# Kernel tuning notes

Measured on AMD Instinct MI355X. Metric: run time of the kernel, lower is better.

Reference implementation:

```python
import jax, jax.numpy as jnp
import numpy as np

EMBED_DIM = 1024
NUM_HEADS = 16
HEAD_DIM = EMBED_DIM // NUM_HEADS
NUM_FEATS = 256
YAT_EPS = 0.1
BATCH = 4
SEQ = 4096


def setup_inputs() -> dict:
    key = jax.random.key(0)
    ks = jax.random.split(key, 6)
    s = 1.0 / np.sqrt(EMBED_DIM)
    return {
        "x": jax.random.normal(ks[0], (BATCH, SEQ, EMBED_DIM), jnp.float32),
        "Wq": jax.random.normal(ks[1], (EMBED_DIM, EMBED_DIM), jnp.float32) * s,
        "bq": jnp.zeros((EMBED_DIM,), jnp.float32),
        "Wk": jax.random.normal(ks[2], (EMBED_DIM, EMBED_DIM), jnp.float32) * s,
        "bk": jnp.zeros((EMBED_DIM,), jnp.float32),
        "Wv": jax.random.normal(ks[3], (EMBED_DIM, EMBED_DIM), jnp.float32) * s,
        "bv": jnp.zeros((EMBED_DIM,), jnp.float32),
        "Wo": jax.random.normal(ks[4], (EMBED_DIM, EMBED_DIM), jnp.float32) * s,
        "bo": jnp.zeros((EMBED_DIM,), jnp.float32),
        "projection": jax.random.normal(ks[5], (NUM_HEADS, NUM_FEATS, HEAD_DIM), jnp.float32),
    }


def _spherical_features(x, projection):
    # x: (b, h, s, d) -> (b, h, s, f)
    x_norm = x / (jnp.linalg.norm(x, axis=-1, keepdims=True) + 1e-8)
    proj = jnp.einsum('bhsd,hfd->bhsf', x_norm, projection)
    return jax.nn.relu(proj) + YAT_EPS


def reference(x, Wq, bq, Wk, bk, Wv, bv, Wo, bo, projection):
    b, s, _ = x.shape
    def heads(t):
        return jnp.transpose(t.reshape(b, s, NUM_HEADS, HEAD_DIM), (0, 2, 1, 3))
    Q = heads(x @ Wq + bq)
    K = heads(x @ Wk + bk)
    V = heads(x @ Wv + bv)
    Qp = _spherical_features(Q, projection)  # (b,h,s,f)
    Kp = _spherical_features(K, projection)
    KV = jnp.einsum('bhsf,bhsd->bhfd', Kp, V)           # (b,h,f,d)
    QKV = jnp.einsum('bhsf,bhfd->bhsd', Qp, KV)          # (b,h,s,d)
    K_sum = jnp.sum(Kp, axis=2)                          # (b,h,f)
    normalizer = jnp.einsum('bhsf,bhf->bhs', Qp, K_sum)[..., None]
    normalizer = jnp.maximum(normalizer, 1e-6)
    out = QKV / normalizer
    out = jnp.transpose(out, (0, 2, 1, 3)).reshape(b, s, EMBED_DIM)
    return out @ Wo + bo
```

## Files before the change

kernel.cpp:

```cpp
#include <hip/hip_runtime.h>
#include <stdint.h>

typedef __bf16 bf16_t;
typedef __bf16 bf16x4 __attribute__((ext_vector_type(4)));
typedef __bf16 bf16x8 __attribute__((ext_vector_type(8)));
typedef float  f32x4  __attribute__((ext_vector_type(4)));

typedef __attribute__((address_space(1))) const uint32_t gas_u32;
typedef __attribute__((address_space(3))) uint32_t las_u32;

#define MFMA16(a, b, c) __builtin_amdgcn_mfma_f32_16x16x32_bf16((a), (b), (c), 0, 0, 0)

__device__ __forceinline__ void gl_lds16(const bf16_t* g, bf16_t* l) {
    __builtin_amdgcn_global_load_lds((gas_u32*)g, (las_u32*)l, 16, 0, 0);
}

__global__ __launch_bounds__(256) void castbf(const float* __restrict__ X,
                                              bf16_t* __restrict__ Xb)
{
    size_t i = ((size_t)blockIdx.x * 256 + threadIdx.x) * 8;
    float4 a = *(const float4*)&X[i];
    float4 b = *(const float4*)&X[i + 4];
    bf16x8 o;
    o[0] = (bf16_t)a.x; o[1] = (bf16_t)a.y; o[2] = (bf16_t)a.z; o[3] = (bf16_t)a.w;
    o[4] = (bf16_t)b.x; o[5] = (bf16_t)b.y; o[6] = (bf16_t)b.z; o[7] = (bf16_t)b.w;
    *(bf16x8*)&Xb[i] = o;
}

__global__ __launch_bounds__(256) void ktrans(
    const float* __restrict__ W0, const float* __restrict__ W1,
    const float* __restrict__ W2, const float* __restrict__ W3,
    bf16_t* __restrict__ WT)
{
    __shared__ float t[64 * 68];
    const int z = blockIdx.z;
    const float* W = (z == 0) ? W0 : (z == 1) ? W1 : (z == 2) ? W2 : W3;
    bf16_t* O = WT + (size_t)z * 1024 * 1024;
    const int r0 = blockIdx.y * 64, c0 = blockIdx.x * 64;
    const int tid = threadIdx.x;
    const int row = tid >> 2, colg = (tid & 3) * 16;
#pragma unroll
    for (int p = 0; p < 4; ++p)
        *(float4*)&t[row * 68 + colg + p * 4] =
            *(const float4*)&W[(size_t)(r0 + row) * 1024 + c0 + colg + p * 4];
    __syncthreads();
    bf16x8 v0, v1;
#pragma unroll
    for (int j = 0; j < 8; ++j) {
        v0[j] = (bf16_t)t[(colg + j) * 68 + row];
        v1[j] = (bf16_t)t[(colg + 8 + j) * 68 + row];
    }
    *(bf16x8*)&O[(size_t)(c0 + row) * 1024 + r0 + colg] = v0;
    *(bf16x8*)&O[(size_t)(c0 + row) * 1024 + r0 + colg + 8] = v1;
}

template <int CMODE, typename OutT>
__global__ __launch_bounds__(256) void gemm_bt(
    const bf16_t* __restrict__ A, const bf16_t* __restrict__ Bt,
    const float* __restrict__ b0, const float* __restrict__ b1,
    const float* __restrict__ b2, OutT* __restrict__ C,
    int M, int N, int K)
{
    __shared__ bf16_t As[128 * 32];
    __shared__ bf16_t Bs[128 * 32];
    __shared__ bf16_t Cs[4][32 * 72];
    const int tid = threadIdx.x;
    const int lane = tid & 63, wave = tid >> 6;
    const int q = lane >> 4, ln = lane & 15;
    const int m0 = blockIdx.x * 128, n0 = blockIdx.y * 128;
    const int wm = (wave >> 1) * 64, wn = (wave & 1) * 64;
    const int srow = tid >> 2, scol = (tid & 3) * 8;

    f32x4 acc[4][4] = {};
    const bf16_t* Ag = A + (size_t)(m0 + srow) * K + scol;
    const bf16_t* Bg = Bt + (size_t)(n0 + srow) * K + scol;
    bf16_t* Al = As + srow * 32 + scol;
    bf16_t* Bl = Bs + srow * 32 + scol;

    for (int k0 = 0; k0 < K; k0 += 32) {
        __syncthreads();
        gl_lds16(Ag + k0, Al);
        gl_lds16(Ag + k0 + (size_t)64 * K, Al + 64 * 32);
        gl_lds16(Bg + k0, Bl);
        gl_lds16(Bg + k0 + (size_t)64 * K, Bl + 64 * 32);
        __syncthreads();
        bf16x8 a[4], b[4];
#pragma unroll
        for (int mt = 0; mt < 4; ++mt)
            a[mt] = *(const bf16x8*)&As[(wm + mt * 16 + ln) * 32 + q * 8];
#pragma unroll
        for (int nt = 0; nt < 4; ++nt)
            b[nt] = *(const bf16x8*)&Bs[(wn + nt * 16 + ln) * 32 + q * 8];
#pragma unroll
        for (int mt = 0; mt < 4; ++mt)
#pragma unroll
            for (int nt = 0; nt < 4; ++nt)
                acc[mt][nt] = MFMA16(a[mt], b[nt], acc[mt][nt]);
    }

    if (CMODE == 0) {
        float* myCf = (float*)&Cs[wave][0];
#pragma unroll
        for (int p = 0; p < 4; ++p) {
#pragma unroll
            for (int nt = 0; nt < 4; ++nt) {
                float bv = b0[n0 + wn + nt * 16 + ln];
#pragma unroll
                for (int r = 0; r < 4; ++r)
                    myCf[(q * 4 + r) * 68 + nt * 16 + ln] = acc[p][nt][r] + bv;
            }
#pragma unroll
            for (int c = 0; c < 4; ++c) {
                int flat = c * 64 + lane;
                int rr = flat >> 4, co = (flat & 15) * 4;
                f32x4 v = *(const f32x4*)&myCf[rr * 68 + co];
                *(f32x4*)&C[(size_t)(m0 + wm + p * 16 + rr) * N + n0 + wn + co] = v;
            }
        }
    } else {
        const int n_first = n0 + wn;
        const int t = n_first >> 10;
        const int h = (n_first >> 6) & 15;
        const float* bp = (t == 0) ? b0 : (t == 1) ? b1 : b2;
        const int m = m0 + wm;
        const int bI = m >> 12, s0 = m & 4095;
        bf16_t* Cp = (bf16_t*)C + (size_t)t * 16777216 + (size_t)(bI * 16 + h) * 262144;
        bf16_t* myCs = &Cs[wave][0];
#pragma unroll
        for (int p = 0; p < 2; ++p) {
#pragma unroll
            for (int mh = 0; mh < 2; ++mh) {
                int mt = p * 2 + mh;
#pragma unroll
                for (int nt = 0; nt < 4; ++nt) {
                    float bv = bp[(n_first + nt * 16 + ln) & 1023];
#pragma unroll
                    for (int r = 0; r < 4; ++r)
                        myCs[(mh * 16 + q * 4 + r) * 72 + nt * 16 + ln] =
                            (bf16_t)(acc[mt][nt][r] + bv);
                }
            }
#pragma unroll
            for (int c = 0; c < 4; ++c) {
                int flat = c * 64 + lane;
                int rr = flat >> 3, co = (flat & 7) * 8;
                bf16x8 v = *(const bf16x8*)&myCs[rr * 72 + co];
                *(bf16x8*)&Cp[(size_t)(s0 + p * 32 + rr) * 64 + co] = v;
            }
        }
    }
}

__global__ __launch_bounds__(256) void kside(
    const bf16_t* __restrict__ Khm, const bf16_t* __restrict__ Vhm,
    const bf16_t* __restrict__ proj, float* __restrict__ P)
{
    __shared__ bf16_t KpT[256 * 72];
    __shared__ bf16_t Vt[80 * 72];
    const int tid = threadIdx.x;
    const int lane = tid & 63, wave = tid >> 6;
    const int q = lane >> 4, ln = lane & 15;
    const int bh = blockIdx.x, c = blockIdx.y;

    const bf16_t* Kh = Khm + (size_t)bh * 262144;
    const bf16_t* Vh = Vhm + (size_t)bh * 262144;
    const bf16_t* pr = proj + (size_t)(bh & 15) * 16384;

    for (int i = tid; i < 16 * 72; i += 256) {
        int rr = i / 72, cc = i % 72;
        Vt[(64 + rr) * 72 + cc] = (rr == 0) ? (bf16_t)1.0f : (bf16_t)0.0f;
    }
    bf16x8 pf[4][2];
#pragma unroll
    for (int nt = 0; nt < 4; ++nt)
#pragma unroll
        for (int ks = 0; ks < 2; ++ks)
            pf[nt][ks] = *(const bf16x8*)&pr[(size_t)(wave * 64 + nt * 16 + ln) * 64 + ks * 32 + q * 8];

    f32x4 kv[4][5] = {};
    const int s_base = c * 512;
    for (int st = 0; st < 8; ++st) {
        const int s0 = s_base + st * 64;
        f32x4 fa[4][4] = {};
#pragma unroll
        for (int mt = 0; mt < 4; ++mt) {
            const bf16_t* rp = &Kh[(size_t)(s0 + mt * 16 + ln) * 64 + q * 8];
            bf16x8 a0 = *(const bf16x8*)rp;
            bf16x8 a1 = *(const bf16x8*)(rp + 32);
            float f[16], ss = 0.f;
#pragma unroll
            for (int i = 0; i < 8; ++i) { f[i] = (float)a0[i]; f[8 + i] = (float)a1[i]; }
#pragma unroll
            for (int i = 0; i < 16; ++i) ss += f[i] * f[i];
            ss += __shfl_xor(ss, 16, 64);
            ss += __shfl_xor(ss, 32, 64);
            float sc = 1.0f / (sqrtf(ss) + 1e-8f);
            bf16x8 na0, na1;
#pragma unroll
            for (int i = 0; i < 8; ++i) {
                na0[i] = (bf16_t)(f[i] * sc);
                na1[i] = (bf16_t)(f[8 + i] * sc);
            }
#pragma unroll
            for (int nt = 0; nt < 4; ++nt) {
                fa[mt][nt] = MFMA16(na0, pf[nt][0], fa[mt][nt]);
                fa[mt][nt] = MFMA16(na1, pf[nt][1], fa[mt][nt]);
            }
        }
        __syncthreads();
#pragma unroll
        for (int mt = 0; mt < 4; ++mt)
#pragma unroll
            for (int nt = 0; nt < 4; ++nt) {
                bf16x4 kp;
#pragma unroll
                for (int r = 0; r < 4; ++r)
                    kp[r] = (bf16_t)(fmaxf(fa[mt][nt][r], 0.0f) + 0.1f);
                *(bf16x4*)&KpT[(wave * 64 + nt * 16 + ln) * 72 + mt * 16 + q * 4] = kp;
            }
        for (int j = tid; j < 512; j += 256) {
            int s = j >> 3, d0 = (j & 7) * 8;
            bf16x8 v = *(const bf16x8*)&Vh[(size_t)(s0 + s) * 64 + d0];
#pragma unroll
            for (int e = 0; e < 8; ++e) Vt[(d0 + e) * 72 + s] = v[e];
        }
        __syncthreads();
#pragma unroll
        for (int ks = 0; ks < 2; ++ks)
#pragma unroll
            for (int mt = 0; mt < 4; ++mt) {
                bf16x8 a = *(const bf16x8*)&KpT[(wave * 64 + mt * 16 + ln) * 72 + ks * 32 + q * 8];
#pragma unroll
                for (int nt = 0; nt < 5; ++nt) {
                    bf16x8 bb = *(const bf16x8*)&Vt[(nt * 16 + ln) * 72 + ks * 32 + q * 8];
                    kv[mt][nt] = MFMA16(a, bb, kv[mt][nt]);
                }
            }
    }
    float* Pp = P + (size_t)(bh * 8 + c) * 65 * 256;
#pragma unroll
    for (int mt = 0; mt < 4; ++mt)
#pragma unroll
        for (int nt = 0; nt < 5; ++nt)
            if (nt < 4 || ln == 0)
                *(f32x4*)&Pp[(size_t)(nt * 16 + ln) * 256 + wave * 64 + mt * 16 + q * 4] = kv[mt][nt];
}

__global__ __launch_bounds__(256) void kreduce(const float* __restrict__ P, bf16_t* __restrict__ KVt)
{
    size_t i = (size_t)blockIdx.x * 256 + threadIdx.x;
    int f = (int)(i & 255);
    int n = (int)((i >> 8) % 80);
    int bh = (int)(i / (256 * 80));
    float s = 0.f;
    if (n < 65) {
        const float* p = P + (size_t)bh * 8 * 65 * 256 + (size_t)n * 256 + f;
#pragma unroll
        for (int c = 0; c < 8; ++c) s += p[(size_t)c * 65 * 256];
    }
    KVt[i] = (bf16_t)s;
}

__global__ __launch_bounds__(256) void qside(
    const bf16_t* __restrict__ Qhm, const bf16_t* __restrict__ proj,
    const bf16_t* __restrict__ KVt, bf16_t* __restrict__ attn)
{
    __shared__ bf16_t Qp[128 * 136];
    const int tid = threadIdx.x;
    const int lane = tid & 63, wave = tid >> 6;
    const int q = lane >> 4, ln = lane & 15;
    const int bh = blockIdx.x, stile = blockIdx.y;
    const int bI = bh >> 4, h = bh & 15;

    const bf16_t* Qh = Qhm + (size_t)bh * 262144 + (size_t)stile * 128 * 64;
    const bf16_t* pr = proj + (size_t)h * 16384;
    const bf16_t* kv = KVt + (size_t)bh * 20480;

    bf16x8 na[2][2];
#pragma unroll
    for (int mt = 0; mt < 2; ++mt) {
        const bf16_t* rp = &Qh[(size_t)(wave * 32 + mt * 16 + ln) * 64 + q * 8];
        bf16x8 a0 = *(const bf16x8*)rp;
        bf16x8 a1 = *(const bf16x8*)(rp + 32);
        float f[16], ss = 0.f;
#pragma unroll
        for (int i = 0; i < 8; ++i) { f[i] = (float)a0[i]; f[8 + i] = (float)a1[i]; }
#pragma unroll
        for (int i = 0; i < 16; ++i) ss += f[i] * f[i];
        ss += __shfl_xor(ss, 16, 64);
        ss += __shfl_xor(ss, 32, 64);
        float sc = 1.0f / (sqrtf(ss) + 1e-8f);
#pragma unroll
        for (int i = 0; i < 8; ++i) {
            na[mt][0][i] = (bf16_t)(f[i] * sc);
            na[mt][1][i] = (bf16_t)(f[8 + i] * sc);
        }
    }

    f32x4 oacc[2][5] = {};
#pragma unroll
    for (int fh = 0; fh < 2; ++fh) {
        f32x4 fa[2][8] = {};
#pragma unroll
        for (int ks = 0; ks < 2; ++ks) {
            bf16x8 bb[8];
#pragma unroll
            for (int nt = 0; nt < 8; ++nt)
                bb[nt] = *(const bf16x8*)&pr[(size_t)(fh * 128 + nt * 16 + ln) * 64 + ks * 32 + q * 8];
#pragma unroll
            for (int mt = 0; mt < 2; ++mt)
#pragma unroll
                for (int nt = 0; nt < 8; ++nt)
                    fa[mt][nt] = MFMA16(na[mt][ks], bb[nt], fa[mt][nt]);
        }
#pragma unroll
        for (int mt = 0; mt < 2; ++mt)
#pragma unroll
            for (int nt = 0; nt < 8; ++nt)
#pragma unroll
                for (int r = 0; r < 4; ++r)
                    Qp[(wave * 32 + mt * 16 + q * 4 + r) * 136 + nt * 16 + ln] =
                        (bf16_t)(fmaxf(fa[mt][nt][r], 0.0f) + 0.1f);
#pragma unroll
        for (int ks = 0; ks < 4; ++ks) {
            bf16x8 aa[2];
#pragma unroll
            for (int mt = 0; mt < 2; ++mt)
                aa[mt] = *(const bf16x8*)&Qp[(wave * 32 + mt * 16 + ln) * 136 + ks * 32 + q * 8];
#pragma unroll
            for (int nt = 0; nt < 5; ++nt) {
                bf16x8 bb = *(const bf16x8*)&kv[(size_t)(nt * 16 + ln) * 256 + fh * 128 + ks * 32 + q * 8];
#pragma unroll
                for (int mt = 0; mt < 2; ++mt)
                    oacc[mt][nt] = MFMA16(aa[mt], bb, oacc[mt][nt]);
            }
        }
    }
    bf16_t* Ap = attn + ((size_t)(bI * 4096 + stile * 128) * 1024) + h * 64;
#pragma unroll
    for (int mt = 0; mt < 2; ++mt)
#pragma unroll
        for (int r = 0; r < 4; ++r) {
            float nrm = fmaxf(__shfl(oacc[mt][4][r], lane & 48, 64), 1e-6f);
            int sl = wave * 32 + mt * 16 + q * 4 + r;
#pragma unroll
            for (int nt = 0; nt < 4; ++nt)
                Ap[(size_t)sl * 1024 + nt * 16 + ln] = (bf16_t)(oacc[mt][nt][r] / nrm);
        }
}

extern "C" void kernel_launch(void* const* d_in, const int* in_sizes, int n_in,
                              void* d_out, int out_size, void* d_ws, size_t ws_size,
                              hipStream_t stream)
{
    const float* x = (const float*)d_in[0];
    const float* Wq = (const float*)d_in[1];
    const float* bq = (const float*)d_in[2];
    const float* Wk = (const float*)d_in[3];
    const float* bk = (const float*)d_in[4];
    const float* Wv = (const float*)d_in[5];
    const float* bv = (const float*)d_in[6];
    const float* Wo = (const float*)d_in[7];
    const float* bo = (const float*)d_in[8];
    const float* proj = (const float*)d_in[9];

    char* ws = (char*)d_ws;
    bf16_t* WT = (bf16_t*)(ws);
    bf16_t* projb = (bf16_t*)(ws + (8ull << 20));
    bf16_t* KVt = (bf16_t*)(ws + (9ull << 20));
    bf16_t* Q = (bf16_t*)(ws + (12ull << 20));
    bf16_t* K = (bf16_t*)(ws + (44ull << 20));
    bf16_t* V = (bf16_t*)(ws + (76ull << 20));
    bf16_t* xb = (bf16_t*)(ws + (108ull << 20));
    float* P = (float*)xb;
    bf16_t* attn = V;
    float* out = (float*)d_out;

    castbf<<<8192, 256, 0, stream>>>(x, xb);
    castbf<<<128, 256, 0, stream>>>(proj, projb);
    ktrans<<<dim3(16, 16, 4), 256, 0, stream>>>(Wq, Wk, Wv, Wo, WT);
    gemm_bt<2, bf16_t><<<dim3(128, 24), 256, 0, stream>>>(
        xb, WT, bq, bk, bv, Q, 16384, 3072, 1024);
    kside<<<dim3(64, 8), 256, 0, stream>>>(K, V, projb, P);
    kreduce<<<5120, 256, 0, stream>>>(P, KVt);
    qside<<<dim3(64, 32), 256, 0, stream>>>(Q, projb, KVt, attn);
    gemm_bt<0, float><<<dim3(128, 8), 256, 0, stream>>>(
        attn, WT + 3ull * 1048576, bo, bo, bo, out, 16384, 1024, 1024);
}
```

Before: 460.9 us.

## Replace GEMM with 256x256-tile double-buffered pipelined kernel using swizzled LDS

Replaces the 128x128 single-buffered bf16 GEMM with a 512-thread kernel computing 256x256 output tiles using K-steps of 64. Global-to-LDS loads are issued in four interleaved stages so the next tiles load while MFMAs run on the current one. The LDS layout is XOR-swizzled to avoid bank conflicts, and s_setprio raises priority around MFMA bursts. This aims to raise operand reuse and hide memory latency in the QKV and output projections, at the cost of 128KB of LDS per block, heavy register use, and fewer blocks in flight.

```diff
diff --git a/kernel.cpp b/kernel.cpp
--- a/kernel.cpp
+++ b/kernel.cpp
@@ -10,6 +10,7 @@
 typedef __attribute__((address_space(3))) uint32_t las_u32;
 
 #define MFMA16(a, b, c) __builtin_amdgcn_mfma_f32_16x16x32_bf16((a), (b), (c), 0, 0, 0)
+#define BAR() asm volatile("s_barrier" ::: "memory")
 
 __device__ __forceinline__ void gl_lds16(const bf16_t* g, bf16_t* l) {
     __builtin_amdgcn_global_load_lds((gas_u32*)g, (las_u32*)l, 16, 0, 0);
@@ -55,89 +56,148 @@
 }
 
 template <int CMODE, typename OutT>
-__global__ __launch_bounds__(256) void gemm_bt(
+__global__ __launch_bounds__(512, 2) void gemm256(
     const bf16_t* __restrict__ A, const bf16_t* __restrict__ Bt,
     const float* __restrict__ b0, const float* __restrict__ b1,
     const float* __restrict__ b2, OutT* __restrict__ C,
     int M, int N, int K)
 {
-    __shared__ bf16_t As[128 * 32];
-    __shared__ bf16_t Bs[128 * 32];
-    __shared__ bf16_t Cs[4][32 * 72];
+    __shared__ bf16_t lds[2][2][256 * 64];
     const int tid = threadIdx.x;
     const int lane = tid & 63, wave = tid >> 6;
     const int q = lane >> 4, ln = lane & 15;
-    const int m0 = blockIdx.x * 128, n0 = blockIdx.y * 128;
-    const int wm = (wave >> 1) * 64, wn = (wave & 1) * 64;
-    const int srow = tid >> 2, scol = (tid & 3) * 8;
-
-    f32x4 acc[4][4] = {};
-    const bf16_t* Ag = A + (size_t)(m0 + srow) * K + scol;
-    const bf16_t* Bg = Bt + (size_t)(n0 + srow) * K + scol;
-    bf16_t* Al = As + srow * 32 + scol;
-    bf16_t* Bl = Bs + srow * 32 + scol;
-
-    for (int k0 = 0; k0 < K; k0 += 32) {
-        __syncthreads();
-        gl_lds16(Ag + k0, Al);
-        gl_lds16(Ag + k0 + (size_t)64 * K, Al + 64 * 32);
-        gl_lds16(Bg + k0, Bl);
-        gl_lds16(Bg + k0 + (size_t)64 * K, Bl + 64 * 32);
-        __syncthreads();
-        bf16x8 a[4], b[4];
-#pragma unroll
-        for (int mt = 0; mt < 4; ++mt)
-            a[mt] = *(const bf16x8*)&As[(wm + mt * 16 + ln) * 32 + q * 8];
-#pragma unroll
-        for (int nt = 0; nt < 4; ++nt)
-            b[nt] = *(const bf16x8*)&Bs[(wn + nt * 16 + ln) * 32 + q * 8];
-#pragma unroll
-        for (int mt = 0; mt < 4; ++mt)
-#pragma unroll
-            for (int nt = 0; nt < 4; ++nt)
-                acc[mt][nt] = MFMA16(a[mt], b[nt], acc[mt][nt]);
-    }
+    const int m0 = blockIdx.x * 256, n0 = blockIdx.y * 256;
+    const int wm = (wave >> 2) * 128, wn = (wave & 3) * 64;
+    const int NT = K >> 6;
+
+    const bf16_t* Ag = A + (size_t)m0 * K;
+    const bf16_t* Bg = Bt + (size_t)n0 * K;
+
+    auto stage = [&](int mat, int half, int tt) {
+        bf16_t* lb = &lds[tt & 1][mat][0];
+        const bf16_t* g = mat ? Bg : Ag;
+        const int k0 = tt << 6;
+#pragma unroll
+        for (int r = 0; r < 2; ++r) {
+            int idx = r * 512 + tid;
+            int ri = idx >> 3;
+            int row = mat ? ((half ? 32 : 0) + (ri & 31) + ((ri & ~31) << 1))
+                          : ((half ? 64 : 0) + (ri & 63) + ((ri & 64) << 1));
+            int gs = (idx & 7) ^ (row & 7);
+            gl_lds16(g + (size_t)row * K + k0 + gs * 8,
+                     lb + row * 64 + (idx & 7) * 8);
+        }
+    };
+
+    bf16x8 aL[4][2], bL0[2][2], bL1[2][2];
+    auto lda = [&](int mh, int cur) {
+#pragma unroll
+        for (int mf = 0; mf < 4; ++mf)
+#pragma unroll
+            for (int ks = 0; ks < 2; ++ks) {
+                int row = wm + (mh * 4 + mf) * 16 + ln;
+                int g = ((ks << 2) + q) ^ (row & 7);
+                aL[mf][ks] = *(const bf16x8*)&lds[cur][0][row * 64 + g * 8];
+            }
+    };
+    auto ldb = [&](bf16x8 (&bL)[2][2], int nh, int cur) {
+#pragma unroll
+        for (int nf = 0; nf < 2; ++nf)
+#pragma unroll
+            for (int ks = 0; ks < 2; ++ks) {
+                int row = wn + (nh * 2 + nf) * 16 + ln;
+                int g = ((ks << 2) + q) ^ (row & 7);
+                bL[nf][ks] = *(const bf16x8*)&lds[cur][1][row * 64 + g * 8];
+            }
+    };
+
+    f32x4 acc[8][4] = {};
+    auto mm = [&](bf16x8 (&bL)[2][2], int mh, int nh) {
+        __builtin_amdgcn_s_setprio(1);
+#pragma unroll
+        for (int mf = 0; mf < 4; ++mf)
+#pragma unroll
+            for (int nf = 0; nf < 2; ++nf)
+#pragma unroll
+                for (int ks = 0; ks < 2; ++ks)
+                    acc[mh * 4 + mf][nh * 2 + nf] =
+                        MFMA16(aL[mf][ks], bL[nf][ks], acc[mh * 4 + mf][nh * 2 + nf]);
+        __builtin_amdgcn_s_setprio(0);
+    };
+
+    stage(0, 0, 0); stage(1, 0, 0); stage(1, 1, 0); stage(0, 1, 0);
+    stage(0, 0, 1); stage(1, 0, 1); stage(1, 1, 1);
+    asm volatile("s_waitcnt vmcnt(6)" ::: "memory");
+    BAR();
+
+    for (int t = 0; t < NT; ++t) {
+        const int cur = t & 1;
+        lda(0, cur); ldb(bL0, 0, cur);
+        if (t + 1 < NT) stage(0, 1, t + 1);
+        BAR();
+        mm(bL0, 0, 0);
+        BAR();
+        ldb(bL1, 1, cur);
+        if (t + 2 < NT) stage(0, 0, t + 2);
+        BAR();
+        mm(bL1, 0, 1);
+        BAR();
+        lda(1, cur);
+        if (t + 2 < NT) stage(1, 0, t + 2);
+        BAR();
+        mm(bL0, 1, 0);
+        BAR();
+        if (t + 2 < NT) stage(1, 1, t + 2);
+        BAR();
+        mm(bL1, 1, 1);
+        if (t + 2 < NT) asm volatile("s_waitcnt vmcnt(6)" ::: "memory");
+        else            asm volatile("s_waitcnt vmcnt(0)" ::: "memory");
+        BAR();
+    }
+    __syncthreads();
 
     if (CMODE == 0) {
-        float* myCf = (float*)&Cs[wave][0];
-#pragma unroll
-        for (int p = 0; p < 4; ++p) {
+        float* myCf = (float*)&lds[0][0][0] + wave * 1088;
+        const int nf0 = n0 + wn;
+        const int mfst = m0 + wm;
+#pragma unroll
+        for (int mt = 0; mt < 8; ++mt) {
 #pragma unroll
             for (int nt = 0; nt < 4; ++nt) {
-                float bv = b0[n0 + wn + nt * 16 + ln];
+                float bv = b0[nf0 + nt * 16 + ln];
 #pragma unroll
                 for (int r = 0; r < 4; ++r)
-                    myCf[(q * 4 + r) * 68 + nt * 16 + ln] = acc[p][nt][r] + bv;
+                    myCf[(q * 4 + r) * 68 + nt * 16 + ln] = acc[mt][nt][r] + bv;
             }
 #pragma unroll
             for (int c = 0; c < 4; ++c) {
                 int flat = c * 64 + lane;
                 int rr = flat >> 4, co = (flat & 15) * 4;
                 f32x4 v = *(const f32x4*)&myCf[rr * 68 + co];
-                *(f32x4*)&C[(size_t)(m0 + wm + p * 16 + rr) * N + n0 + wn + co] = v;
+                *(f32x4*)&C[(size_t)(mfst + mt * 16 + rr) * N + nf0 + co] = v;
             }
         }
     } else {
+        bf16_t* myCs = &lds[0][0][0] + wave * 2304;
         const int n_first = n0 + wn;
-        const int t = n_first >> 10;
+        const int t_ = n_first >> 10;
         const int h = (n_first >> 6) & 15;
-        const float* bp = (t == 0) ? b0 : (t == 1) ? b1 : b2;
-        const int m = m0 + wm;
-        const int bI = m >> 12, s0 = m & 4095;
-        bf16_t* Cp = (bf16_t*)C + (size_t)t * 16777216 + (size_t)(bI * 16 + h) * 262144;
-        bf16_t* myCs = &Cs[wave][0];
-#pragma unroll
-        for (int p = 0; p < 2; ++p) {
-#pragma unroll
-            for (int mh = 0; mh < 2; ++mh) {
-                int mt = p * 2 + mh;
+        const float* bp = (t_ == 0) ? b0 : (t_ == 1) ? b1 : b2;
+        const int m_first = m0 + wm;
+        const int bI = m_first >> 12, s0 = m_first & 4095;
+        bf16_t* Cp = (bf16_t*)C + (size_t)t_ * 16777216 + (size_t)(bI * 16 + h) * 262144;
+#pragma unroll
+        for (int p = 0; p < 4; ++p) {
+#pragma unroll
+            for (int mh2 = 0; mh2 < 2; ++mh2) {
+                int mf = p * 2 + mh2;
 #pragma unroll
                 for (int nt = 0; nt < 4; ++nt) {
                     float bv = bp[(n_first + nt * 16 + ln) & 1023];
 #pragma unroll
                     for (int r = 0; r < 4; ++r)
-                        myCs[(mh * 16 + q * 4 + r) * 72 + nt * 16 + ln] =
-                            (bf16_t)(acc[mt][nt][r] + bv);
+                        myCs[(mh2 * 16 + q * 4 + r) * 72 + nt * 16 + ln] =
+                            (bf16_t)(acc[mf][nt][r] + bv);
                 }
             }
 #pragma unroll
@@ -379,11 +439,11 @@
     castbf<<<8192, 256, 0, stream>>>(x, xb);
     castbf<<<128, 256, 0, stream>>>(proj, projb);
     ktrans<<<dim3(16, 16, 4), 256, 0, stream>>>(Wq, Wk, Wv, Wo, WT);
-    gemm_bt<2, bf16_t><<<dim3(128, 24), 256, 0, stream>>>(
+    gemm256<2, bf16_t><<<dim3(64, 12), 512, 0, stream>>>(
         xb, WT, bq, bk, bv, Q, 16384, 3072, 1024);
     kside<<<dim3(64, 8), 256, 0, stream>>>(K, V, projb, P);
     kreduce<<<5120, 256, 0, stream>>>(P, KVt);
     qside<<<dim3(64, 32), 256, 0, stream>>>(Q, projb, KVt, attn);
-    gemm_bt<0, float><<<dim3(128, 8), 256, 0, stream>>>(
+    gemm256<0, float><<<dim3(64, 4), 512, 0, stream>>>(
         attn, WT + 3ull * 1048576, bo, bo, bo, out, 16384, 1024, 1024);
 }
```

After: 422.6 us. 1.09x faster.
